# Optimization experiments

Measured on AMD Instinct MI355X. Metric: run time of the kernel, lower is better.

## Reference

```python
import jax, jax.numpy as jnp
import numpy as np

NKV = 8      # n_head_kv
G = 8        # n_head // n_head_kv
D = 64       # head_dim (hardcoded in source views)
NH = NKV * G # n_head = 64


def rotate_half(x):
    x1, x2 = x[..., : D // 2], x[..., D // 2:]
    return jnp.concatenate((-x2, x1), axis=-1)


def setup_inputs() -> dict:
    key = jax.random.key(0)
    ks = jax.random.split(key, 9)
    B, S, H = 2, 1024, 4096
    hidden_states = jax.random.normal(ks[0], (B, S, H), dtype=jnp.float32)
    alibi = jnp.zeros((B * NH, 1, S), dtype=jnp.float32)            # unused in this forward path
    attention_mask = jnp.zeros((B, 1, S, S), dtype=jnp.float32)      # unused (is_causal=True)
    cos = jax.random.uniform(ks[1], (S, D), dtype=jnp.float32, minval=-1.0, maxval=1.0)
    sin = jax.random.uniform(ks[2], (S, D), dtype=jnp.float32, minval=-1.0, maxval=1.0)
    wq = jax.random.normal(ks[3], (H, H), dtype=jnp.float32) * 0.02          # Linear weight (out, in)
    wk = jax.random.normal(ks[4], (NKV * D, H), dtype=jnp.float32) * 0.02
    wv = jax.random.normal(ks[5], (NKV * D, H), dtype=jnp.float32) * 0.02
    wd = jax.random.normal(ks[6], (H, H), dtype=jnp.float32) * 0.02          # dense weight
    return {"hidden_states": hidden_states, "alibi": alibi, "attention_mask": attention_mask,
            "cos": cos, "sin": sin, "wq": wq, "wk": wk, "wv": wv, "wd": wd}


def reference(hidden_states, alibi, attention_mask, cos, sin, wq, wk, wv, wd):
    B, S, H = hidden_states.shape
    # fused-style projections (Linear: x @ W.T, no bias)
    # q: [B, S, NKV, G, D] -> [B, NKV, G, S, D]; head h = kv_group*G + j (group-major, matches source rearrange)
    q = (hidden_states @ wq.T).reshape(B, S, NKV, G, D).transpose(0, 2, 3, 1, 4)
    k = (hidden_states @ wk.T).reshape(B, S, NKV, D).transpose(0, 2, 1, 3)   # [B, NKV, S, D]
    v = (hidden_states @ wv.T).reshape(B, S, NKV, D).transpose(0, 2, 1, 3)
    # RoPE (cos/sin broadcast over batch/head dims)
    q = q * cos + rotate_half(q) * sin
    k = k * cos + rotate_half(k) * sin
    # grouped-query attention without materializing broadcast K/V
    inv_norm = jnp.asarray(1.0 / np.sqrt(D), dtype=hidden_states.dtype)
    scores = jnp.einsum('bkgsd,bktd->bkgst', q, k) * inv_norm        # [B, NKV, G, S, S]
    causal = jnp.tril(jnp.ones((S, S), dtype=bool))
    neg = jnp.finfo(scores.dtype).min
    scores = jnp.where(causal, scores, scores + neg)
    probs = jax.nn.softmax(scores, axis=-1)
    out = jnp.einsum('bkgst,bktd->bkgsd', probs, v)                  # [B, NKV, G, S, D]
    out = out.reshape(B, NH, S, D).transpose(0, 2, 1, 3).reshape(B, S, NH * D)
    return out @ wd.T
```

## Files before the change

### kernel.cpp

```cpp
#include <hip/hip_runtime.h>
#include <hip/hip_bf16.h>
#include <cstdint>

typedef short short8 __attribute__((ext_vector_type(8)));
typedef __bf16 bf16x8 __attribute__((ext_vector_type(8)));
typedef float float4v __attribute__((ext_vector_type(4)));
typedef float float16v __attribute__((ext_vector_type(16)));

#define NKV 8
#define G 8
#define D 64
#define NH 64
#define BB 2
#define S 1024
#define H 4096
#define MROWS (BB*S)
#define NQKV (H + 2*NKV*D)

__device__ __forceinline__ unsigned short f2b(float f) {
    union { float f; uint32_t u; } v; v.f = f;
    uint32_t u = v.u;
    uint32_t r = (u + 0x7FFFu + ((u >> 16) & 1u)) >> 16;
    return (unsigned short)r;
}
__device__ __forceinline__ float b2f(unsigned short b) {
    union { float f; uint32_t u; } v; v.u = ((uint32_t)b) << 16;
    return v.f;
}
__device__ __forceinline__ unsigned short f2b_n(float f) {
    union { __bf16 h; unsigned short u; } v; v.h = (__bf16)f;
    return v.u;
}

__device__ __forceinline__ void gload_lds16(const unsigned short* g, unsigned short* l) {
    __builtin_amdgcn_global_load_lds(
        (const __attribute__((address_space(1))) uint32_t*)g,
        (__attribute__((address_space(3))) uint32_t*)l, 16, 0, 0);
}

__global__ void cvt_all(const float* __restrict__ hs, const float* __restrict__ wq,
                        const float* __restrict__ wk, const float* __restrict__ wv,
                        const float* __restrict__ wd,
                        unsigned short* __restrict__ hs_b, unsigned short* __restrict__ wqkv_b,
                        unsigned short* __restrict__ wd_b) {
    const size_t N0 = (size_t)MROWS * H;
    const size_t N1 = (size_t)H * H;
    const size_t N2 = (size_t)512 * H;
    const size_t N3 = (size_t)512 * H;
    const size_t N4 = (size_t)H * H;
    const size_t total4 = (N0 + N1 + N2 + N3 + N4) / 4;
    size_t i = (size_t)blockIdx.x * blockDim.x + threadIdx.x;
    const size_t stride = (size_t)gridDim.x * blockDim.x;
    for (; i < total4; i += stride) {
        size_t e = i * 4;
        const float* s; unsigned short* d;
        if (e < N0)                { s = hs + e;                  d = hs_b + e; }
        else if (e < N0+N1)        { s = wq + (e-N0);             d = wqkv_b + (e-N0); }
        else if (e < N0+N1+N2)     { s = wk + (e-N0-N1);          d = wqkv_b + N1 + (e-N0-N1); }
        else if (e < N0+N1+N2+N3)  { s = wv + (e-N0-N1-N2);       d = wqkv_b + N1+N2 + (e-N0-N1-N2); }
        else                       { s = wd + (e-N0-N1-N2-N3);    d = wd_b + (e-N0-N1-N2-N3); }
        float4 f = *(const float4*)s;
        ushort4 o;
        o.x = f2b(f.x); o.y = f2b(f.y); o.z = f2b(f.z); o.w = f2b(f.w);
        *(ushort4*)d = o;
    }
}

template <int MODE>
__global__ __launch_bounds__(256) void gemm_nt(
    const unsigned short* __restrict__ A, const unsigned short* __restrict__ W,
    void* __restrict__ Cv, int M, int N, int K,
    const float* __restrict__ cosb, const float* __restrict__ sinb,
    unsigned short* __restrict__ qa, unsigned short* __restrict__ ka,
    unsigned short* __restrict__ vt) {
    __shared__ unsigned short sh[17408];
    unsigned short* As = sh;
    unsigned short* Bs = sh + 4096;
    const int bm = blockIdx.y * 128, bn = blockIdx.x * 128;
    const int tid = threadIdx.x;
    const int w = tid >> 6, lane = tid & 63;
    const int n32 = lane & 31, khalf = lane >> 5;
    const int wm = (w & 1) * 64, wn = (w >> 1) * 64;

    const int r0 = tid >> 2;
    const int c0 = (tid & 3) ^ ((r0 >> 2) & 3);
    const unsigned short* pA0 = A + (size_t)(bm + r0) * K + c0 * 8;
    const unsigned short* pA1 = A + (size_t)(bm + r0 + 64) * K + c0 * 8;
    const unsigned short* pW0 = W + (size_t)(bn + r0) * K + c0 * 8;
    const unsigned short* pW1 = W + (size_t)(bn + r0 + 64) * K + c0 * 8;
    unsigned short* Asl0 = As + tid * 8;
    unsigned short* Asl1 = As + 2048 + tid * 8;
    unsigned short* Bsl0 = Bs + tid * 8;
    unsigned short* Bsl1 = Bs + 2048 + tid * 8;

    const unsigned short* aP[2][2];
    const unsigned short* bP[2][2];
#pragma unroll
    for (int g = 0; g < 2; g++)
#pragma unroll
        for (int s = 0; s < 2; s++) {
            int cp = ((s << 1) | khalf) ^ ((n32 >> 2) & 3);
            aP[g][s] = &As[(wm + g * 32 + n32) * 32 + cp * 8];
            bP[g][s] = &Bs[(wn + g * 32 + n32) * 32 + cp * 8];
        }

    float16v acc[2][2] = {};

    const int iters = K >> 5;
    for (int it = 0; it < iters; ++it) {
        __syncthreads();
        gload_lds16(pA0, Asl0);
        gload_lds16(pA1, Asl1);
        gload_lds16(pW0, Bsl0);
        gload_lds16(pW1, Bsl1);
        pA0 += 32; pA1 += 32; pW0 += 32; pW1 += 32;
        __syncthreads();
        bf16x8 af[2][2], bf[2][2];
#pragma unroll
        for (int g = 0; g < 2; g++)
#pragma unroll
            for (int s = 0; s < 2; s++) {
                af[g][s] = *(const bf16x8*)aP[g][s];
                bf[g][s] = *(const bf16x8*)bP[g][s];
            }
#pragma unroll
        for (int s = 0; s < 2; s++)
#pragma unroll
            for (int mg = 0; mg < 2; mg++)
#pragma unroll
                for (int ng = 0; ng < 2; ng++)
                    acc[mg][ng] = __builtin_amdgcn_mfma_f32_32x32x16_bf16(
                        af[mg][s], bf[ng][s], acc[mg][ng], 0, 0, 0);
    }

    if (MODE == 0) {
#pragma unroll
        for (int mg = 0; mg < 2; mg++) {
#pragma unroll
            for (int ng = 0; ng < 2; ng++) {
                int gcol = bn + wn + ng * 32 + n32;
#pragma unroll
                for (int reg = 0; reg < 16; reg++) {
                    int grow = bm + wm + mg * 32 + (reg & 3) + 8 * (reg >> 2) + 4 * khalf;
                    ((float*)Cv)[(size_t)grow * N + gcol] = acc[mg][ng][reg];
                }
            }
        }
    } else {
        const int colbase = bn + wn;
        const float SCQ = 0.125f * 1.44269504089f;
        if (bn < H + 512) {
#pragma unroll
            for (int mg = 0; mg < 2; mg++) {
#pragma unroll
                for (int reg = 0; reg < 16; reg++) {
                    int grow = bm + wm + mg * 32 + (reg & 3) + 8 * (reg >> 2) + 4 * khalf;
                    int s = grow & 1023, b = grow >> 10;
                    float x0 = acc[mg][0][reg], x1 = acc[mg][1][reg];
                    float c0  = cosb[s * 64 + n32],      sn0 = sinb[s * 64 + n32];
                    float c1  = cosb[s * 64 + 32 + n32], sn1 = sinb[s * 64 + 32 + n32];
                    float y0 = x0 * c0 - x1 * sn0;
                    float y1 = x1 * c1 + x0 * sn1;
                    unsigned short* dp;
                    if (bn < H) {
                        y0 *= SCQ; y1 *= SCQ;
                        dp = qa + (size_t)(b * 64 + (colbase >> 6)) * (S * D) + s * 64 + n32;
                    } else {
                        dp = ka + (size_t)(b * 8 + ((colbase - H) >> 6)) * (S * D) + s * 64 + n32;
                    }
                    dp[0] = f2b(y0); dp[32] = f2b(y1);
                }
            }
        } else {
            __syncthreads();
#pragma unroll
            for (int mg = 0; mg < 2; mg++)
#pragma unroll
                for (int ng = 0; ng < 2; ng++)
#pragma unroll
                    for (int reg = 0; reg < 16; reg++) {
                        int cl = wn + ng * 32 + n32;
                        int rl = wm + mg * 32 + (reg & 3) + 8 * (reg >> 2) + 4 * khalf;
                        sh[cl * 136 + rl] = f2b(acc[mg][ng][reg]);
                    }
            __syncthreads();
            {
                const int bb = bm >> 10, s0 = bm & 1023;
                const int kv0 = (bn - (H + 512)) >> 6;
                const int cl = tid >> 1, shalf = (tid & 1) * 64;
                const int kv = kv0 + (cl >> 6), dd = cl & 63;
                unsigned short* dstp = vt + (size_t)(bb * 8 + kv) * (D * S)
                                          + (size_t)dd * S + s0 + shalf;
                const unsigned short* srcp = sh + cl * 136 + shalf;
#pragma unroll
                for (int j = 0; j < 8; j++)
                    *(short8*)(dstp + j * 8) = *(const short8*)(srcp + j * 8);
            }
        }
    }
}

__global__ __launch_bounds__(256, 2) void attn_kernel(
    const unsigned short* __restrict__ qa, const unsigned short* __restrict__ ka,
    const unsigned short* __restrict__ vt, unsigned short* __restrict__ out) {
    __shared__ unsigned short KV[2][8192];
    __shared__ unsigned short Ps[4 * 16 * 72];
    const int p = blockIdx.x;
    const int yy = blockIdx.y;
    const int b = yy >> 5, kvh = (yy >> 2) & 7, gp = yy & 3;
    const int h0 = b * 64 + kvh * 8 + gp * 2;
    const int tid = threadIdx.x, w = tid >> 6, lane = tid & 63;
    const int col = lane & 15, quad = lane >> 4;
    const unsigned short* Kg = ka + (size_t)(b * NKV + kvh) * (S * D);
    const unsigned short* Vg = vt + (size_t)(b * NKV + kvh) * (D * S);
    float4v zero4 = {0.f, 0.f, 0.f, 0.f};

    const int sr = tid >> 3;
    const int scs = ((tid & 7) ^ (sr & 7)) * 8;

#define ATTN_STAGE(BUF, KB) { \
    gload_lds16(Kg + (size_t)((KB) + sr) * 64 + scs,      &KV[BUF][tid * 8]); \
    gload_lds16(Kg + (size_t)((KB) + sr + 32) * 64 + scs, &KV[BUF][2048 + tid * 8]); \
    gload_lds16(Vg + (size_t)sr * S + (KB) + scs,         &KV[BUF][4096 + tid * 8]); \
    gload_lds16(Vg + (size_t)(sr + 32) * S + (KB) + scs,  &KV[BUF][6144 + tid * 8]); }

    const int qt0 = p, qt1 = 15 - p;
    const int qb[2] = {qt0 * 64, qt1 * 64};

    bf16x8 aq[2][2][2];
#pragma unroll
    for (int part = 0; part < 2; part++)
#pragma unroll
        for (int hd = 0; hd < 2; hd++)
#pragma unroll
            for (int c = 0; c < 2; c++)
                aq[part][hd][c] = *(const bf16x8*)&qa[(size_t)(h0 + hd) * (S * D)
                                    + (size_t)qb[part] * D + (w * 16 + col) * 64 + c * 32 + quad * 8];

    float l_run[2][2][4] = {};
    float4v o_acc[2][2][4];
#pragma unroll
    for (int part = 0; part < 2; part++)
#pragma unroll
        for (int hd = 0; hd < 2; hd++)
#pragma unroll
            for (int dg = 0; dg < 4; dg++) o_acc[part][hd][dg] = zero4;

    ATTN_STAGE(0, 0)
    asm volatile("s_waitcnt vmcnt(0)" ::: "memory");
    __builtin_amdgcn_s_barrier();

    for (int kt = 0; kt <= qt1; kt++) {
        const int cur = kt & 1;
        const int knext = ((kt < qt1) ? kt + 1 : qt1) * 64;
        ATTN_STAGE(cur ^ 1, knext)
        asm volatile("s_waitcnt vmcnt(4)" ::: "memory");
        __builtin_amdgcn_s_barrier();
        __builtin_amdgcn_sched_barrier(0);

        const unsigned short* Kl = KV[cur];
        const unsigned short* Vl = KV[cur] + 4096;
        bf16x8 bk[4][2], bv[4][2];
#pragma unroll
        for (int n16 = 0; n16 < 4; n16++) {
            const int R = n16 * 16 + col, x = R & 7;
            bk[n16][0] = *(const bf16x8*)&Kl[R * 64 + (quad ^ x) * 8];
            bk[n16][1] = *(const bf16x8*)&Kl[R * 64 + ((quad + 4) ^ x) * 8];
        }
#pragma unroll
        for (int dg = 0; dg < 4; dg++) {
            const int R = dg * 16 + col, x = R & 7;
            bv[dg][0] = *(const bf16x8*)&Vl[R * 64 + (quad ^ x) * 8];
            bv[dg][1] = *(const bf16x8*)&Vl[R * 64 + ((quad + 4) ^ x) * 8];
        }

#pragma unroll
        for (int part = 0; part < 2; part++) {
            const int qtp = part ? qt1 : qt0;
            if (kt > qtp) continue;
#pragma unroll
            for (int hd = 0; hd < 2; hd++) {
                float4v sc[4];
                __builtin_amdgcn_s_setprio(1);
#pragma unroll
                for (int n16 = 0; n16 < 4; n16++) {
                    float4v a = __builtin_amdgcn_mfma_f32_16x16x32_bf16(aq[part][hd][0], bk[n16][0], zero4, 0, 0, 0);
                    sc[n16] = __builtin_amdgcn_mfma_f32_16x16x32_bf16(aq[part][hd][1], bk[n16][1], a, 0, 0, 0);
                }
                __builtin_amdgcn_s_setprio(0);
                if (kt == qtp) {
#pragma unroll
                    for (int n16 = 0; n16 < 4; n16++) {
                        int keyl = n16 * 16 + col;
#pragma unroll
                        for (int r = 0; r < 4; r++) {
                            int qrl = w * 16 + quad * 4 + r;
                            sc[n16][r] = (keyl <= qrl) ? sc[n16][r] : -1e30f;
                        }
                    }
                }
#pragma unroll
                for (int n16 = 0; n16 < 4; n16++)
#pragma unroll
                    for (int r = 0; r < 4; r++) {
                        float pr = __builtin_amdgcn_exp2f(sc[n16][r]);
                        sc[n16][r] = pr;
                        l_run[part][hd][r] += pr;
                        Ps[w * 1152 + (quad * 4 + r) * 72 + n16 * 16 + col] = f2b_n(pr);
                    }
                bf16x8 ap[2];
#pragma unroll
                for (int c = 0; c < 2; c++)
                    ap[c] = *(const bf16x8*)&Ps[w * 1152 + col * 72 + c * 32 + quad * 8];
                __builtin_amdgcn_s_setprio(1);
#pragma unroll
                for (int dg = 0; dg < 4; dg++) {
                    float4v t = __builtin_amdgcn_mfma_f32_16x16x32_bf16(ap[0], bv[dg][0], o_acc[part][hd][dg], 0, 0, 0);
                    o_acc[part][hd][dg] = __builtin_amdgcn_mfma_f32_16x16x32_bf16(ap[1], bv[dg][1], t, 0, 0, 0);
                }
                __builtin_amdgcn_s_setprio(0);
            }
        }
        __builtin_amdgcn_sched_barrier(0);
        __builtin_amdgcn_s_barrier();
    }

#pragma unroll
    for (int part = 0; part < 2; part++)
#pragma unroll
        for (int hd = 0; hd < 2; hd++) {
            const int hcol = ((h0 + hd) & 63) * 64;
#pragma unroll
            for (int r = 0; r < 4; r++) {
                float lsum = l_run[part][hd][r];
#pragma unroll
                for (int off = 1; off < 16; off <<= 1) lsum += __shfl_xor(lsum, off);
                float inv = 1.f / lsum;
                int grow = b * S + qb[part] + w * 16 + quad * 4 + r;
#pragma unroll
                for (int dg = 0; dg < 4; dg++)
                    out[(size_t)grow * H + hcol + dg * 16 + col] = f2b_n(o_acc[part][hd][dg][r] * inv);
            }
        }
#undef ATTN_STAGE
}

extern "C" void kernel_launch(void* const* d_in, const int* in_sizes, int n_in,
                              void* d_out, int out_size, void* d_ws, size_t ws_size,
                              hipStream_t stream) {
    const float* hs   = (const float*)d_in[0];
    const float* cosb = (const float*)d_in[3];
    const float* sinb = (const float*)d_in[4];
    const float* wq   = (const float*)d_in[5];
    const float* wk   = (const float*)d_in[6];
    const float* wv   = (const float*)d_in[7];
    const float* wd   = (const float*)d_in[8];

    char* p = (char*)d_ws;
    auto alloc = [&](size_t bytes) { char* r = p; p += (bytes + 255) & ~(size_t)255; return r; };
    unsigned short* wqkv_b = (unsigned short*)alloc((size_t)NQKV * H * 2);
    unsigned short* wd_b   = (unsigned short*)alloc((size_t)H * H * 2);
    unsigned short* qa     = (unsigned short*)alloc((size_t)BB * NH * S * D * 2);
    unsigned short* ka     = (unsigned short*)alloc((size_t)BB * NKV * S * D * 2);
    unsigned short* vt     = (unsigned short*)alloc((size_t)BB * NKV * S * D * 2);
    unsigned short* hs_b   = (unsigned short*)alloc((size_t)MROWS * H * 2);
    unsigned short* ao     = hs_b;

    cvt_all<<<4096, 256, 0, stream>>>(hs, wq, wk, wv, wd, hs_b, wqkv_b, wd_b);

    gemm_nt<1><<<dim3(NQKV / 128, MROWS / 128), 256, 0, stream>>>(
        hs_b, wqkv_b, nullptr, MROWS, NQKV, H, cosb, sinb, qa, ka, vt);
    attn_kernel<<<dim3(8, 64), 256, 0, stream>>>(qa, ka, vt, ao);
    gemm_nt<0><<<dim3(H / 128, MROWS / 128), 256, 0, stream>>>(
        ao, wd_b, d_out, MROWS, H, H, nullptr, nullptr, nullptr, nullptr, nullptr);
}
```

Before: 443.2 us.

## Split-K the output projection with atomic adds and swizzle GEMM block order

The dense output GEMM is split into two K halves along a new grid z dimension. Partial results are combined with float atomic adds into an output that is first zeroed with a memset. Block indices are also remapped with an XCD-style swizzle, so consecutive workgroups go to the same chiplet to improve L2 reuse. This doubles the number of workgroups for the 512-tile grid, at the cost of atomic traffic, an extra memset over the output, and a floating-point summation order that is no longer deterministic.

```diff
diff --git a/kernel.cpp b/kernel.cpp
--- a/kernel.cpp
+++ b/kernel.cpp
@@ -69,14 +69,25 @@
 template <int MODE>
 __global__ __launch_bounds__(256) void gemm_nt(
     const unsigned short* __restrict__ A, const unsigned short* __restrict__ W,
-    void* __restrict__ Cv, int M, int N, int K,
+    void* __restrict__ Cv, int M, int N, int K, int ksplit,
     const float* __restrict__ cosb, const float* __restrict__ sinb,
     unsigned short* __restrict__ qa, unsigned short* __restrict__ ka,
     unsigned short* __restrict__ vt) {
     __shared__ unsigned short sh[17408];
     unsigned short* As = sh;
     unsigned short* Bs = sh + 4096;
-    const int bm = blockIdx.y * 128, bn = blockIdx.x * 128;
+
+    const int gx = gridDim.x, gy = gridDim.y;
+    const int nwg = gx * gy * gridDim.z;
+    const int orig = blockIdx.x + gx * (blockIdx.y + gy * blockIdx.z);
+    const int swz = (orig & 7) * (nwg >> 3) + (orig >> 3);
+    const int bx = swz % gx;
+    const int rem = swz / gx;
+    const int by = rem % gy, bz = rem / gy;
+
+    const int bm = by * 128, bn = bx * 128;
+    const int Kloc = K / ksplit;
+    const int k0 = bz * Kloc;
     const int tid = threadIdx.x;
     const int w = tid >> 6, lane = tid & 63;
     const int n32 = lane & 31, khalf = lane >> 5;
@@ -84,10 +95,10 @@
 
     const int r0 = tid >> 2;
     const int c0 = (tid & 3) ^ ((r0 >> 2) & 3);
-    const unsigned short* pA0 = A + (size_t)(bm + r0) * K + c0 * 8;
-    const unsigned short* pA1 = A + (size_t)(bm + r0 + 64) * K + c0 * 8;
-    const unsigned short* pW0 = W + (size_t)(bn + r0) * K + c0 * 8;
-    const unsigned short* pW1 = W + (size_t)(bn + r0 + 64) * K + c0 * 8;
+    const unsigned short* pA0 = A + (size_t)(bm + r0) * K + k0 + c0 * 8;
+    const unsigned short* pA1 = A + (size_t)(bm + r0 + 64) * K + k0 + c0 * 8;
+    const unsigned short* pW0 = W + (size_t)(bn + r0) * K + k0 + c0 * 8;
+    const unsigned short* pW1 = W + (size_t)(bn + r0 + 64) * K + k0 + c0 * 8;
     unsigned short* Asl0 = As + tid * 8;
     unsigned short* Asl1 = As + 2048 + tid * 8;
     unsigned short* Bsl0 = Bs + tid * 8;
@@ -106,7 +117,7 @@
 
     float16v acc[2][2] = {};
 
-    const int iters = K >> 5;
+    const int iters = Kloc >> 5;
     for (int it = 0; it < iters; ++it) {
         __syncthreads();
         gload_lds16(pA0, Asl0);
@@ -142,7 +153,7 @@
 #pragma unroll
                 for (int reg = 0; reg < 16; reg++) {
                     int grow = bm + wm + mg * 32 + (reg & 3) + 8 * (reg >> 2) + 4 * khalf;
-                    ((float*)Cv)[(size_t)grow * N + gcol] = acc[mg][ng][reg];
+                    unsafeAtomicAdd(&((float*)Cv)[(size_t)grow * N + gcol], acc[mg][ng][reg]);
                 }
             }
         }
@@ -366,11 +377,13 @@
     unsigned short* hs_b   = (unsigned short*)alloc((size_t)MROWS * H * 2);
     unsigned short* ao     = hs_b;
 
+    hipMemsetAsync(d_out, 0, (size_t)MROWS * H * sizeof(float), stream);
+
     cvt_all<<<4096, 256, 0, stream>>>(hs, wq, wk, wv, wd, hs_b, wqkv_b, wd_b);
 
     gemm_nt<1><<<dim3(NQKV / 128, MROWS / 128), 256, 0, stream>>>(
-        hs_b, wqkv_b, nullptr, MROWS, NQKV, H, cosb, sinb, qa, ka, vt);
+        hs_b, wqkv_b, nullptr, MROWS, NQKV, H, 1, cosb, sinb, qa, ka, vt);
     attn_kernel<<<dim3(8, 64), 256, 0, stream>>>(qa, ka, vt, ao);
-    gemm_nt<0><<<dim3(H / 128, MROWS / 128), 256, 0, stream>>>(
-        ao, wd_b, d_out, MROWS, H, H, nullptr, nullptr, nullptr, nullptr, nullptr);
-}
+    gemm_nt<0><<<dim3(H / 128, MROWS / 128, 2), 256, 0, stream>>>(
+        ao, wd_b, d_out, MROWS, H, H, 2, nullptr, nullptr, nullptr, nullptr, nullptr);
+}
```

Result: slower. 550.8 us (+24.3%).

## Double-buffer GEMM LDS tiles to overlap global loads with MFMA compute

Applied to the files above, without the earlier changes.

Replaces the single-buffered K-loop in the bf16 GEMM with a two-stage ping-pong pipeline. The next K-tile is loaded into the alternate LDS buffer while MFMAs run on the current one, with explicit vmcnt waits and barriers. This hides global-to-LDS latency that previously stalled every iteration behind two syncthreads. It uses 32KB of the existing shared array and issues a redundant final prefetch of the last tile to keep the loop branch-free.

```diff
diff --git a/kernel.cpp b/kernel.cpp
--- a/kernel.cpp
+++ b/kernel.cpp
@@ -66,6 +66,37 @@
     }
 }
 
+#define STAGE_G(BUF, T) { \
+    const size_t ko = (size_t)(T) * 32; \
+    gload_lds16(gA0 + ko, sh + (BUF) * 8192 + tid * 8); \
+    gload_lds16(gA1 + ko, sh + (BUF) * 8192 + 2048 + tid * 8); \
+    gload_lds16(gW0 + ko, sh + 4096 + (BUF) * 8192 + tid * 8); \
+    gload_lds16(gW1 + ko, sh + 4096 + (BUF) * 8192 + 2048 + tid * 8); }
+#define GCOMPUTE(BUF) { \
+    bf16x8 af[2][2], bf[2][2]; \
+    _Pragma("unroll") \
+    for (int g = 0; g < 2; g++) \
+    _Pragma("unroll") \
+    for (int s = 0; s < 2; s++) { \
+        af[g][s] = *(const bf16x8*)(aP[g][s] + (BUF) * 8192); \
+        bf[g][s] = *(const bf16x8*)(bP[g][s] + (BUF) * 8192); } \
+    _Pragma("unroll") \
+    for (int s = 0; s < 2; s++) \
+    _Pragma("unroll") \
+    for (int mg = 0; mg < 2; mg++) \
+    _Pragma("unroll") \
+    for (int ng = 0; ng < 2; ng++) \
+        acc[mg][ng] = __builtin_amdgcn_mfma_f32_32x32x16_bf16( \
+            af[mg][s], bf[ng][s], acc[mg][ng], 0, 0, 0); }
+#define GPIPE(BUF, T) \
+    STAGE_G((BUF) ^ 1, T) \
+    asm volatile("s_waitcnt vmcnt(4)" ::: "memory"); \
+    __builtin_amdgcn_s_barrier(); \
+    __builtin_amdgcn_sched_barrier(0); \
+    GCOMPUTE(BUF) \
+    __builtin_amdgcn_sched_barrier(0); \
+    __builtin_amdgcn_s_barrier();
+
 template <int MODE>
 __global__ __launch_bounds__(256) void gemm_nt(
     const unsigned short* __restrict__ A, const unsigned short* __restrict__ W,
@@ -74,8 +105,6 @@
     unsigned short* __restrict__ qa, unsigned short* __restrict__ ka,
     unsigned short* __restrict__ vt) {
     __shared__ unsigned short sh[17408];
-    unsigned short* As = sh;
-    unsigned short* Bs = sh + 4096;
     const int bm = blockIdx.y * 128, bn = blockIdx.x * 128;
     const int tid = threadIdx.x;
     const int w = tid >> 6, lane = tid & 63;
@@ -84,14 +113,10 @@
 
     const int r0 = tid >> 2;
     const int c0 = (tid & 3) ^ ((r0 >> 2) & 3);
-    const unsigned short* pA0 = A + (size_t)(bm + r0) * K + c0 * 8;
-    const unsigned short* pA1 = A + (size_t)(bm + r0 + 64) * K + c0 * 8;
-    const unsigned short* pW0 = W + (size_t)(bn + r0) * K + c0 * 8;
-    const unsigned short* pW1 = W + (size_t)(bn + r0 + 64) * K + c0 * 8;
-    unsigned short* Asl0 = As + tid * 8;
-    unsigned short* Asl1 = As + 2048 + tid * 8;
-    unsigned short* Bsl0 = Bs + tid * 8;
-    unsigned short* Bsl1 = Bs + 2048 + tid * 8;
+    const unsigned short* gA0 = A + (size_t)(bm + r0) * K + c0 * 8;
+    const unsigned short* gA1 = A + (size_t)(bm + r0 + 64) * K + c0 * 8;
+    const unsigned short* gW0 = W + (size_t)(bn + r0) * K + c0 * 8;
+    const unsigned short* gW1 = W + (size_t)(bn + r0 + 64) * K + c0 * 8;
 
     const unsigned short* aP[2][2];
     const unsigned short* bP[2][2];
@@ -100,37 +125,22 @@
 #pragma unroll
         for (int s = 0; s < 2; s++) {
             int cp = ((s << 1) | khalf) ^ ((n32 >> 2) & 3);
-            aP[g][s] = &As[(wm + g * 32 + n32) * 32 + cp * 8];
-            bP[g][s] = &Bs[(wn + g * 32 + n32) * 32 + cp * 8];
+            aP[g][s] = &sh[(wm + g * 32 + n32) * 32 + cp * 8];
+            bP[g][s] = &sh[4096 + (wn + g * 32 + n32) * 32 + cp * 8];
         }
 
     float16v acc[2][2] = {};
 
     const int iters = K >> 5;
-    for (int it = 0; it < iters; ++it) {
-        __syncthreads();
-        gload_lds16(pA0, Asl0);
-        gload_lds16(pA1, Asl1);
-        gload_lds16(pW0, Bsl0);
-        gload_lds16(pW1, Bsl1);
-        pA0 += 32; pA1 += 32; pW0 += 32; pW1 += 32;
-        __syncthreads();
-        bf16x8 af[2][2], bf[2][2];
-#pragma unroll
-        for (int g = 0; g < 2; g++)
-#pragma unroll
-            for (int s = 0; s < 2; s++) {
-                af[g][s] = *(const bf16x8*)aP[g][s];
-                bf[g][s] = *(const bf16x8*)bP[g][s];
-            }
-#pragma unroll
-        for (int s = 0; s < 2; s++)
-#pragma unroll
-            for (int mg = 0; mg < 2; mg++)
-#pragma unroll
-                for (int ng = 0; ng < 2; ng++)
-                    acc[mg][ng] = __builtin_amdgcn_mfma_f32_32x32x16_bf16(
-                        af[mg][s], bf[ng][s], acc[mg][ng], 0, 0, 0);
+    STAGE_G(0, 0)
+    asm volatile("s_waitcnt vmcnt(0)" ::: "memory");
+    __builtin_amdgcn_s_barrier();
+
+    for (int it = 0; it < iters; it += 2) {
+        const int t1 = it + 1;
+        const int t2 = (it + 2 < iters) ? it + 2 : iters - 1;
+        GPIPE(0, t1)
+        GPIPE(1, t2)
     }
 
     if (MODE == 0) {
```

After: 439.7 us. About the same (-0.8%).

## Overlap dense weight bf16 conversion with QKV GEMM main loop

Applied to the files above, without the earlier changes.

Removes the dense weight conversion from the standalone conversion kernel. Each thread of the QKV projection GEMM now converts a strided slice of the dense weight to bf16 every fourth K iteration. The aim is to hide this bandwidth-bound conversion behind the compute-bound GEMM instead of running it serially. It adds global traffic and registers inside the GEMM loop, which could slow the MFMA pipeline.

```diff
diff --git a/kernel.cpp b/kernel.cpp
--- a/kernel.cpp
+++ b/kernel.cpp
@@ -40,15 +40,12 @@
 
 __global__ void cvt_all(const float* __restrict__ hs, const float* __restrict__ wq,
                         const float* __restrict__ wk, const float* __restrict__ wv,
-                        const float* __restrict__ wd,
-                        unsigned short* __restrict__ hs_b, unsigned short* __restrict__ wqkv_b,
-                        unsigned short* __restrict__ wd_b) {
+                        unsigned short* __restrict__ hs_b, unsigned short* __restrict__ wqkv_b) {
     const size_t N0 = (size_t)MROWS * H;
     const size_t N1 = (size_t)H * H;
     const size_t N2 = (size_t)512 * H;
     const size_t N3 = (size_t)512 * H;
-    const size_t N4 = (size_t)H * H;
-    const size_t total4 = (N0 + N1 + N2 + N3 + N4) / 4;
+    const size_t total4 = (N0 + N1 + N2 + N3) / 4;
     size_t i = (size_t)blockIdx.x * blockDim.x + threadIdx.x;
     const size_t stride = (size_t)gridDim.x * blockDim.x;
     for (; i < total4; i += stride) {
@@ -57,8 +54,7 @@
         if (e < N0)                { s = hs + e;                  d = hs_b + e; }
         else if (e < N0+N1)        { s = wq + (e-N0);             d = wqkv_b + (e-N0); }
         else if (e < N0+N1+N2)     { s = wk + (e-N0-N1);          d = wqkv_b + N1 + (e-N0-N1); }
-        else if (e < N0+N1+N2+N3)  { s = wv + (e-N0-N1-N2);       d = wqkv_b + N1+N2 + (e-N0-N1-N2); }
-        else                       { s = wd + (e-N0-N1-N2-N3);    d = wd_b + (e-N0-N1-N2-N3); }
+        else                       { s = wv + (e-N0-N1-N2);       d = wqkv_b + N1+N2 + (e-N0-N1-N2); }
         float4 f = *(const float4*)s;
         ushort4 o;
         o.x = f2b(f.x); o.y = f2b(f.y); o.z = f2b(f.z); o.w = f2b(f.w);
@@ -72,7 +68,8 @@
     void* __restrict__ Cv, int M, int N, int K,
     const float* __restrict__ cosb, const float* __restrict__ sinb,
     unsigned short* __restrict__ qa, unsigned short* __restrict__ ka,
-    unsigned short* __restrict__ vt) {
+    unsigned short* __restrict__ vt,
+    const float* __restrict__ wdsrc, unsigned short* __restrict__ wddst) {
     __shared__ unsigned short sh[17408];
     unsigned short* As = sh;
     unsigned short* Bs = sh + 4096;
@@ -93,6 +90,9 @@
     unsigned short* Bsl0 = Bs + tid * 8;
     unsigned short* Bsl1 = Bs + 2048 + tid * 8;
 
+    const size_t cvtbase = (size_t)(blockIdx.y * gridDim.x + blockIdx.x) * 256 + tid;
+    const size_t NWD4 = (size_t)H * H / 4;
+
     const unsigned short* aP[2][2];
     const unsigned short* bP[2][2];
 #pragma unroll
@@ -114,6 +114,17 @@
         gload_lds16(pW0, Bsl0);
         gload_lds16(pW1, Bsl1);
         pA0 += 32; pA1 += 32; pW0 += 32; pW1 += 32;
+        if (MODE == 1) {
+            if ((it & 3) == 0) {
+                size_t idx = cvtbase + (size_t)(it >> 2) * 163840;
+                if (idx < NWD4) {
+                    float4 f = ((const float4*)wdsrc)[idx];
+                    ushort4 o;
+                    o.x = f2b(f.x); o.y = f2b(f.y); o.z = f2b(f.z); o.w = f2b(f.w);
+                    ((ushort4*)wddst)[idx] = o;
+                }
+            }
+        }
         __syncthreads();
         bf16x8 af[2][2], bf[2][2];
 #pragma unroll
@@ -366,11 +377,12 @@
     unsigned short* hs_b   = (unsigned short*)alloc((size_t)MROWS * H * 2);
     unsigned short* ao     = hs_b;
 
-    cvt_all<<<4096, 256, 0, stream>>>(hs, wq, wk, wv, wd, hs_b, wqkv_b, wd_b);
+    cvt_all<<<4096, 256, 0, stream>>>(hs, wq, wk, wv, hs_b, wqkv_b);
 
     gemm_nt<1><<<dim3(NQKV / 128, MROWS / 128), 256, 0, stream>>>(
-        hs_b, wqkv_b, nullptr, MROWS, NQKV, H, cosb, sinb, qa, ka, vt);
+        hs_b, wqkv_b, nullptr, MROWS, NQKV, H, cosb, sinb, qa, ka, vt, wd, wd_b);
     attn_kernel<<<dim3(8, 64), 256, 0, stream>>>(qa, ka, vt, ao);
     gemm_nt<0><<<dim3(H / 128, MROWS / 128), 256, 0, stream>>>(
-        ao, wd_b, d_out, MROWS, H, H, nullptr, nullptr, nullptr, nullptr, nullptr);
-}
+        ao, wd_b, d_out, MROWS, H, H, nullptr, nullptr, nullptr, nullptr, nullptr,
+        nullptr, nullptr);
+}
```

New measurement: 459.7 us. +3.7%, slower.
